# Kernel optimization log

Measured on AMD Instinct MI355X. Metric: run time of the kernel, lower is better.

The kernel has to match this reference:

```python
import jax, jax.numpy as jnp
import numpy as np

T = 0.07  # softmax temperature from __init__
N_QUEUES = 4


def _l2norm(x, axis):
    return x / jnp.maximum(jnp.linalg.norm(x, axis=axis, keepdims=True), 1e-12)


def setup_inputs() -> dict:
    key = jax.random.key(0)
    k1, k2, k3, k4, k5, k6 = jax.random.split(key, 6)
    N, D_in, dim, K = 512, 2048, 128, 65536
    im_q = jax.random.normal(k1, (N, D_in), dtype=jnp.float32)
    im_k = jax.random.normal(k2, (N, D_in), dtype=jnp.float32)
    W_q = jax.random.normal(k3, (D_in, dim), dtype=jnp.float32) * (1.0 / np.sqrt(D_in))
    W_k = jax.random.normal(k4, (D_in, dim), dtype=jnp.float32) * (1.0 / np.sqrt(D_in))
    queues = jax.random.normal(k5, (N_QUEUES, dim, K), dtype=jnp.float32)
    queues = _l2norm(queues, axis=1)  # normalize along feature dim, as in __init__
    label = jax.random.randint(k6, (N,), 0, 4, dtype=jnp.int32)
    return {"im_q": im_q, "im_k": im_k, "W_q": W_q, "W_k": W_k,
            "queues": queues, "label": label}


def reference(im_q, im_k, W_q, W_k, queues, label):
    # encoder_q / encoder_k abstracted as linear projections
    q = _l2norm(im_q @ W_q, axis=1)                      # [N, C]
    k = _l2norm(im_k @ W_k, axis=1)                      # [N, C] (no_grad in original)
    l_pos = jnp.einsum('nc,nc->n', q, k)[:, None]        # [N, 1]
    # per-sample queue routing: queue index = (label - 1) % 4
    route = jnp.mod(label - 1, N_QUEUES)                 # [N]
    onehot = jax.nn.one_hot(route, N_QUEUES, dtype=q.dtype)  # [N, G]
    # l_neg[n, k] = sum_c q[n, c] * queues[route[n], c, k], as grouped matmul
    l_neg = jnp.einsum('ngc,gck->nk', q[:, None, :] * onehot[:, :, None], queues)  # [N, K]
    logits = jnp.concatenate([l_pos, l_neg], axis=1) / T  # [N, 1+K]
    labels = jnp.zeros(logits.shape[0], dtype=jnp.int32)
    return logits, labels
```

## Files before the change

### kernel.cpp

```cpp
#include <hip/hip_runtime.h>

typedef short short8 __attribute__((ext_vector_type(8)));
typedef float floatx4 __attribute__((ext_vector_type(4)));

__device__ __forceinline__ unsigned short f2bf(float f) {
  unsigned u = __float_as_uint(f);
  u += 0x7FFFu + ((u >> 16) & 1u);
  return (unsigned short)(u >> 16);
}

__global__ __launch_bounds__(512, 4) void proj_partial(
    const float* __restrict__ im_q, const float* __restrict__ im_k,
    const float* __restrict__ Wq, const float* __restrict__ Wk,
    float* __restrict__ part, int* __restrict__ cnt) {
  __shared__ float imS[16 * 260];
  const int t = threadIdx.x;
  if (blockIdx.x == 0 && blockIdx.y == 0 && blockIdx.z == 0 && t < 4) cnt[t] = 0;
  const int which = blockIdx.z;
  const float* __restrict__ im = which ? im_k : im_q;
  const float* __restrict__ W  = which ? Wk : Wq;
  const int d0 = blockIdx.x * 256;
  const int row0 = blockIdx.y * 16;
#pragma unroll
  for (int p = 0; p < 2; ++p) {
    const int idx = t + p * 512;
    const int r = idx >> 6;
    const int dd = (idx & 63) * 4;
    *(float4*)(imS + r * 260 + dd) =
        *(const float4*)(im + (size_t)(row0 + r) * 2048 + d0 + dd);
  }
  __syncthreads();
  const int c4 = (t & 31) * 4;
  const int r  = t >> 5;
  float acc0 = 0.f, acc1 = 0.f, acc2 = 0.f, acc3 = 0.f;
  const float* __restrict__ Wp = W + (size_t)d0 * 128 + c4;
#pragma unroll 8
  for (int d = 0; d < 256; ++d) {
    const float4 w = *(const float4*)(Wp + (size_t)d * 128);
    const float a = imS[r * 260 + d];
    acc0 += a * w.x; acc1 += a * w.y; acc2 += a * w.z; acc3 += a * w.w;
  }
  *(float4*)(part + ((size_t)(which * 8 + blockIdx.x) * 512 + row0 + r) * 128 + c4) =
      make_float4(acc0, acc1, acc2, acc3);
}

__global__ __launch_bounds__(128) void finalize(
    const float* __restrict__ part, const int* __restrict__ label,
    unsigned short* __restrict__ qbf, int* __restrict__ cnt,
    int* __restrict__ rows, float* __restrict__ out) {
  const int n = blockIdx.x, c = threadIdx.x;
  float qraw = 0.f, kraw = 0.f;
#pragma unroll
  for (int ch = 0; ch < 8; ++ch) {
    qraw += part[((size_t)ch * 512 + n) * 128 + c];
    kraw += part[((size_t)(8 + ch) * 512 + n) * 128 + c];
  }
  float sq = qraw * qraw, sk = kraw * kraw, dt = qraw * kraw;
#pragma unroll
  for (int off = 32; off > 0; off >>= 1) {
    sq += __shfl_down(sq, off, 64);
    sk += __shfl_down(sk, off, 64);
    dt += __shfl_down(dt, off, 64);
  }
  __shared__ float sh[3][2];
  const int lane = c & 63, wv = c >> 6;
  if (lane == 0) { sh[0][wv] = sq; sh[1][wv] = sk; sh[2][wv] = dt; }
  __syncthreads();
  const float tsq = sh[0][0] + sh[0][1];
  const float tsk = sh[1][0] + sh[1][1];
  const float tdt = sh[2][0] + sh[2][1];
  const float nq = fmaxf(sqrtf(tsq), 1e-12f);
  const float nk = fmaxf(sqrtf(tsk), 1e-12f);
  qbf[n * 128 + c] = f2bf(qraw / nq);
  if (c == 0) {
    out[(size_t)n * 65537] = tdt / (nq * nk) * (1.0f / 0.07f);
    ((int*)out)[(size_t)512 * 65537 + n] = 0;
    int g = ((label[n] - 1) % 4 + 4) % 4;
    int pos = atomicAdd(cnt + g, 1);
    rows[g * 512 + pos] = n;
  }
}

__global__ __launch_bounds__(256, 3) void moco_lneg(
    const float* __restrict__ queues, const unsigned short* __restrict__ qbf,
    const int* __restrict__ cnt, const int* __restrict__ rows,
    float* __restrict__ out) {
  __shared__ int rowsS[512];
  const int g = blockIdx.y;
  const int Mg = cnt[g];
  if (Mg == 0) return;
  const int t = threadIdx.x;
  for (int i = t; i < 512; i += 256) rowsS[i] = rows[g * 512 + i];
  const int lane = t & 63, wave = t >> 6;
  const int qd = lane >> 4, l16 = lane & 15;
  const int j0 = blockIdx.x * 128;
  short8 bf[4][2];
  {
    const float* __restrict__ qb =
        queues + ((size_t)(g * 128 + qd * 8)) * 65536 + j0 + l16;
#pragma unroll
    for (int kk = 0; kk < 4; ++kk) {
#pragma unroll
      for (int s = 0; s < 2; ++s) {
        const float* __restrict__ p =
            qb + (size_t)(kk * 32) * 65536 + (wave * 2 + s) * 16;
        float f[8];
#pragma unroll
        for (int e = 0; e < 8; ++e) f[e] = p[(size_t)e * 65536];
        unsigned* d = (unsigned*)&bf[kk][s];
#pragma unroll
        for (int i = 0; i < 4; ++i)
          d[i] = (unsigned)f2bf(f[2 * i]) | ((unsigned)f2bf(f[2 * i + 1]) << 16);
      }
    }
  }
  __syncthreads();
  const float invT = 1.0f / 0.07f;
  const int nch = (Mg + 127) >> 7;
  for (int ch = 0; ch < nch; ++ch) {
    const int valid = min(Mg - ch * 128, 128);
    floatx4 acc[8][2];
#pragma unroll
    for (int rb = 0; rb < 8; ++rb) {
      floatx4 z = {0.f, 0.f, 0.f, 0.f};
      acc[rb][0] = z; acc[rb][1] = z;
    }
    __builtin_amdgcn_s_setprio(1);
#pragma unroll
    for (int rb = 0; rb < 8; ++rb) {
      if (rb * 16 < valid) {
        const int m = rb * 16 + l16;
        const int n = (m < valid) ? rowsS[ch * 128 + m] : 0;
        const unsigned short* __restrict__ ap = qbf + (size_t)n * 128 + qd * 8;
#pragma unroll
        for (int kk = 0; kk < 4; ++kk) {
          const short8 afrag = *(const short8*)(ap + kk * 32);
          acc[rb][0] = __builtin_amdgcn_mfma_f32_16x16x32_bf16(afrag, bf[kk][0], acc[rb][0], 0, 0, 0);
          acc[rb][1] = __builtin_amdgcn_mfma_f32_16x16x32_bf16(afrag, bf[kk][1], acc[rb][1], 0, 0, 0);
        }
      }
    }
    __builtin_amdgcn_s_setprio(0);
#pragma unroll
    for (int rb = 0; rb < 8; ++rb) {
      if (rb * 16 < valid) {
#pragma unroll
        for (int r = 0; r < 4; ++r) {
          const int ml = rb * 16 + qd * 4 + r;
          if (ml < valid) {
            const size_t base = (size_t)rowsS[ch * 128 + ml] * 65537 + 1 + j0;
            out[base + (wave * 2 + 0) * 16 + l16] = acc[rb][0][r] * invT;
            out[base + (wave * 2 + 1) * 16 + l16] = acc[rb][1][r] * invT;
          }
        }
      }
    }
  }
}

extern "C" void kernel_launch(void* const* d_in, const int* in_sizes, int n_in,
                              void* d_out, int out_size, void* d_ws, size_t ws_size,
                              hipStream_t stream) {
  const float* im_q   = (const float*)d_in[0];
  const float* im_k   = (const float*)d_in[1];
  const float* Wq     = (const float*)d_in[2];
  const float* Wk     = (const float*)d_in[3];
  const float* queues = (const float*)d_in[4];
  const int*   label  = (const int*)d_in[5];
  float* out = (float*)d_out;

  char* ws = (char*)d_ws;
  float* part = (float*)ws;
  unsigned short* qbf = (unsigned short*)(ws + (4u << 20));
  int* cnt  = (int*)(ws + (4u << 20) + (128u << 10));
  int* rows = cnt + 4;

  proj_partial<<<dim3(8, 32, 2), 512, 0, stream>>>(im_q, im_k, Wq, Wk, part, cnt);
  finalize<<<512, 128, 0, stream>>>(part, label, qbf, cnt, rows, out);
  moco_lneg<<<dim3(512, 4), 256, 0, stream>>>(queues, qbf, cnt, rows, out);
}
```

Baseline: 330.1 us.

## Prepack gathered query rows into MFMA fragment layout and double column tiles per block

Adds a qpack kernel that gathers routed query rows per queue group into a contiguous, zero-padded MFMA A-fragment layout in workspace, replacing per-lane indirect row gathers in the main GEMM with coalesced 16-byte loads. The l_neg kernel now processes two 128-column queue tiles per block with half the grid and lower occupancy hint, and handles rows beyond the first 128 in a separate simpler loop. This removes indirection and scattered A loads but adds a kernel launch and reuses the partial-sum workspace region for the packed buffer.

Result: no change. 334.0 us (+1.2%).

```diff
diff --git a/kernel.cpp b/kernel.cpp
--- a/kernel.cpp
+++ b/kernel.cpp
@@ -81,8 +81,31 @@
   }
 }
 
-__global__ __launch_bounds__(256, 3) void moco_lneg(
-    const float* __restrict__ queues, const unsigned short* __restrict__ qbf,
+__global__ __launch_bounds__(256) void qpack(
+    const unsigned short* __restrict__ qbf, const int* __restrict__ cnt,
+    const int* __restrict__ rows, unsigned short* __restrict__ Apack) {
+  const int g = blockIdx.x >> 2, ch = blockIdx.x & 3;
+  const int Mg = cnt[g];
+  const int t = threadIdx.x;
+#pragma unroll
+  for (int w = 0; w < 8; ++w) {
+    const int slot = w * 256 + t;
+    const int kk = slot >> 9;
+    const int rb = (slot >> 6) & 7;
+    const int lane = slot & 63;
+    const int l16 = lane & 15, qd = lane >> 4;
+    const int m = ch * 128 + rb * 16 + l16;
+    uint4 v = make_uint4(0u, 0u, 0u, 0u);
+    if (m < Mg) {
+      const int n = rows[g * 512 + m];
+      v = *(const uint4*)(qbf + (size_t)n * 128 + kk * 32 + qd * 8);
+    }
+    *(uint4*)(Apack + ((size_t)blockIdx.x * 2048 + slot) * 8) = v;
+  }
+}
+
+__global__ __launch_bounds__(256, 2) void moco_lneg(
+    const float* __restrict__ queues, const unsigned short* __restrict__ Apack,
     const int* __restrict__ cnt, const int* __restrict__ rows,
     float* __restrict__ out) {
   __shared__ int rowsS[512];
@@ -91,34 +114,36 @@
   if (Mg == 0) return;
   const int t = threadIdx.x;
   for (int i = t; i < 512; i += 256) rowsS[i] = rows[g * 512 + i];
+  __syncthreads();
   const int lane = t & 63, wave = t >> 6;
   const int qd = lane >> 4, l16 = lane & 15;
-  const int j0 = blockIdx.x * 128;
-  short8 bf[4][2];
-  {
-    const float* __restrict__ qb =
-        queues + ((size_t)(g * 128 + qd * 8)) * 65536 + j0 + l16;
-#pragma unroll
-    for (int kk = 0; kk < 4; ++kk) {
-#pragma unroll
-      for (int s = 0; s < 2; ++s) {
-        const float* __restrict__ p =
-            qb + (size_t)(kk * 32) * 65536 + (wave * 2 + s) * 16;
-        float f[8];
-#pragma unroll
-        for (int e = 0; e < 8; ++e) f[e] = p[(size_t)e * 65536];
-        unsigned* d = (unsigned*)&bf[kk][s];
-#pragma unroll
-        for (int i = 0; i < 4; ++i)
-          d[i] = (unsigned)f2bf(f[2 * i]) | ((unsigned)f2bf(f[2 * i + 1]) << 16);
-      }
-    }
-  }
-  __syncthreads();
   const float invT = 1.0f / 0.07f;
-  const int nch = (Mg + 127) >> 7;
-  for (int ch = 0; ch < nch; ++ch) {
-    const int valid = min(Mg - ch * 128, 128);
+  const int valid0 = min(Mg, 128);
+  const unsigned short* __restrict__ Ab =
+      Apack + (size_t)g * 4 * 16384 + (size_t)lane * 8;
+
+  for (int jt = 0; jt < 2; ++jt) {
+    const int j0 = (blockIdx.x * 2 + jt) * 128;
+    short8 bf[4][2];
+    {
+      const float* __restrict__ qb =
+          queues + ((size_t)(g * 128 + qd * 8)) * 65536 + j0 + l16;
+#pragma unroll
+      for (int kk = 0; kk < 4; ++kk) {
+#pragma unroll
+        for (int s = 0; s < 2; ++s) {
+          const float* __restrict__ p =
+              qb + (size_t)(kk * 32) * 65536 + (wave * 2 + s) * 16;
+          float f[8];
+#pragma unroll
+          for (int e = 0; e < 8; ++e) f[e] = p[(size_t)e * 65536];
+          unsigned* d = (unsigned*)&bf[kk][s];
+#pragma unroll
+          for (int i = 0; i < 4; ++i)
+            d[i] = (unsigned)f2bf(f[2 * i]) | ((unsigned)f2bf(f[2 * i + 1]) << 16);
+        }
+      }
+    }
     floatx4 acc[8][2];
 #pragma unroll
     for (int rb = 0; rb < 8; ++rb) {
@@ -128,13 +153,10 @@
     __builtin_amdgcn_s_setprio(1);
 #pragma unroll
     for (int rb = 0; rb < 8; ++rb) {
-      if (rb * 16 < valid) {
-        const int m = rb * 16 + l16;
-        const int n = (m < valid) ? rowsS[ch * 128 + m] : 0;
-        const unsigned short* __restrict__ ap = qbf + (size_t)n * 128 + qd * 8;
+      if (rb * 16 < valid0) {
 #pragma unroll
         for (int kk = 0; kk < 4; ++kk) {
-          const short8 afrag = *(const short8*)(ap + kk * 32);
+          const short8 afrag = *(const short8*)(Ab + kk * 4096 + rb * 512);
           acc[rb][0] = __builtin_amdgcn_mfma_f32_16x16x32_bf16(afrag, bf[kk][0], acc[rb][0], 0, 0, 0);
           acc[rb][1] = __builtin_amdgcn_mfma_f32_16x16x32_bf16(afrag, bf[kk][1], acc[rb][1], 0, 0, 0);
         }
@@ -143,15 +165,36 @@
     __builtin_amdgcn_s_setprio(0);
 #pragma unroll
     for (int rb = 0; rb < 8; ++rb) {
-      if (rb * 16 < valid) {
+      if (rb * 16 < valid0) {
 #pragma unroll
         for (int r = 0; r < 4; ++r) {
           const int ml = rb * 16 + qd * 4 + r;
-          if (ml < valid) {
-            const size_t base = (size_t)rowsS[ch * 128 + ml] * 65537 + 1 + j0;
+          if (ml < valid0) {
+            const size_t base = (size_t)rowsS[ml] * 65537 + 1 + j0;
             out[base + (wave * 2 + 0) * 16 + l16] = acc[rb][0][r] * invT;
             out[base + (wave * 2 + 1) * 16 + l16] = acc[rb][1][r] * invT;
           }
+        }
+      }
+    }
+    for (int mb = 8; mb * 16 < Mg; ++mb) {
+      const int chh = mb >> 3, rbi = mb & 7;
+      const unsigned short* __restrict__ At =
+          Apack + ((size_t)(g * 4 + chh) * 2048 + (size_t)lane) * 8;
+      floatx4 a0 = {0.f, 0.f, 0.f, 0.f}, a1 = {0.f, 0.f, 0.f, 0.f};
+#pragma unroll
+      for (int kk = 0; kk < 4; ++kk) {
+        const short8 afrag = *(const short8*)(At + kk * 4096 + rbi * 512);
+        a0 = __builtin_amdgcn_mfma_f32_16x16x32_bf16(afrag, bf[kk][0], a0, 0, 0, 0);
+        a1 = __builtin_amdgcn_mfma_f32_16x16x32_bf16(afrag, bf[kk][1], a1, 0, 0, 0);
+      }
+#pragma unroll
+      for (int r = 0; r < 4; ++r) {
+        const int ml = mb * 16 + qd * 4 + r;
+        if (ml < Mg) {
+          const size_t base = (size_t)rowsS[ml] * 65537 + 1 + j0;
+          out[base + (wave * 2 + 0) * 16 + l16] = a0[r] * invT;
+          out[base + (wave * 2 + 1) * 16 + l16] = a1[r] * invT;
         }
       }
     }
@@ -174,8 +217,10 @@
   unsigned short* qbf = (unsigned short*)(ws + (4u << 20));
   int* cnt  = (int*)(ws + (4u << 20) + (128u << 10));
   int* rows = cnt + 4;
+  unsigned short* Apack = (unsigned short*)ws;
 
   proj_partial<<<dim3(8, 32, 2), 512, 0, stream>>>(im_q, im_k, Wq, Wk, part, cnt);
   finalize<<<512, 128, 0, stream>>>(part, label, qbf, cnt, rows, out);
-  moco_lneg<<<dim3(512, 4), 256, 0, stream>>>(queues, qbf, cnt, rows, out);
-}
+  qpack<<<16, 256, 0, stream>>>(qbf, cnt, rows, Apack);
+  moco_lneg<<<dim3(256, 4), 256, 0, stream>>>(queues, Apack, cnt, rows, out);
+}
```
